# Kernel optimization log

Measured on AMD Instinct MI355X. Metric: run time of the kernel, lower is better.

Reference implementation:

```python
import jax, jax.numpy as jnp
import numpy as np

N = 8192
FIN = 128
FOUT = 64
NEG_BIG = -9e15


def setup_inputs() -> dict:
    key = jax.random.key(0)
    k1, k2, k3, k4 = jax.random.split(key, 4)
    x = jax.random.normal(k1, (N, FIN), dtype=jnp.float32)
    adj = jax.random.randint(k2, (N, N), 0, 2, dtype=jnp.int32)
    stdv_w = 1.0 / np.sqrt(FOUT)
    W = jax.random.uniform(k3, (FIN, FOUT), dtype=jnp.float32, minval=-stdv_w, maxval=stdv_w)
    # weight2: stdv = 1/sqrt(1) = 1
    a = jax.random.uniform(k4, (2 * FOUT, 1), dtype=jnp.float32, minval=-1.0, maxval=1.0)
    return {"x": x, "adj": adj, "W": W, "a": a}


def reference(x, adj, W, a):
    # h = x W  -> [N, Fout]
    h = x @ W
    # e_ij = relu(a^T [h_i || h_j]) decomposed exactly: a1.h_i + a2.h_j
    a1 = a[:FOUT, 0]  # [Fout]
    a2 = a[FOUT:, 0]  # [Fout]
    s1 = h @ a1  # [N]
    s2 = h @ a2  # [N]
    e = jax.nn.relu(s1[:, None] + s2[None, :])  # [N, N]
    att_logits = jnp.where(adj > 0, e, jnp.float32(NEG_BIG))
    attention = jax.nn.softmax(att_logits, axis=-1)  # [N, N]
    # dropout omitted (eval mode / p applied only in training)
    out = attention @ h  # [N, Fout]
    return out[None]  # [1, N, Fout] matching batch_size=1 reshape
```

## Files before the change

### kernel.cpp

```cpp
#include <hip/hip_runtime.h>
#include <cstdint>
#include <cstddef>

#define NN 8192
#define FIN 128
#define FOUT 64
#define BM 32
#define BN 64
#define JSPLIT 4
#define JCH (NN / JSPLIT)
#define NCHUNK (JCH / BN)
#define LDP 72

typedef __bf16 bf16x8 __attribute__((ext_vector_type(8)));
typedef unsigned short u16x8 __attribute__((ext_vector_type(8)));
typedef float f32x4 __attribute__((ext_vector_type(4)));

__device__ __forceinline__ unsigned short f2bf(float f) {
    unsigned u = __float_as_uint(f);
    u += 0x7FFFu + ((u >> 16) & 1u);
    return (unsigned short)(u >> 16);
}
__device__ __forceinline__ float bf2f(unsigned short b) {
    return __uint_as_float(((unsigned)b) << 16);
}

__global__ __launch_bounds__(256) void gat_prep(
    const float* __restrict__ x, const float* __restrict__ W,
    const float* __restrict__ a, float* __restrict__ s1,
    float* __restrict__ s2, unsigned short* __restrict__ Ht,
    unsigned int* __restrict__ s2max_enc)
{
    __shared__ __align__(16) float Wt[FOUT][FIN + 4];
    __shared__ float wa1[FIN], wa2[FIN];
    __shared__ float ash[2 * FOUT];
    __shared__ float s2sh[BM];

    const int tid = threadIdx.x;
    const int i0 = blockIdx.x * BM;

    for (int it = 0; it < 32; ++it) {
        int idx = it * 256 + tid;
        int k = idx >> 6, t = idx & 63;
        Wt[t][k] = W[idx];
    }
    if (tid < 2 * FOUT) ash[tid] = a[tid];
    __syncthreads();

    if (tid < FIN) {
        int k = tid;
        float acc = 0.f;
        #pragma unroll 8
        for (int t = 0; t < FOUT; ++t) acc = fmaf(Wt[t][k], ash[t], acc);
        wa1[k] = acc;
    } else {
        int k = tid - FIN;
        float acc = 0.f;
        #pragma unroll 8
        for (int t = 0; t < FOUT; ++t) acc = fmaf(Wt[t][k], ash[FOUT + t], acc);
        wa2[k] = acc;
    }
    __syncthreads();

    {
        int r = tid >> 3;
        int seg = tid & 7;
        const float* xp = x + (size_t)(i0 + r) * FIN + seg * 16;
        float d1 = 0.f, d2 = 0.f;
        #pragma unroll
        for (int m = 0; m < 16; ++m) {
            float xv = xp[m];
            d1 = fmaf(xv, wa1[seg * 16 + m], d1);
            d2 = fmaf(xv, wa2[seg * 16 + m], d2);
        }
        #pragma unroll
        for (int mk = 1; mk < 8; mk <<= 1) {
            d1 += __shfl_xor(d1, mk);
            d2 += __shfl_xor(d2, mk);
        }
        if (seg == 0) {
            s1[i0 + r] = d1;
            s2[i0 + r] = d2;
            s2sh[r] = d2;
        }
    }

    {
        const int lane = tid & 63;
        const int wv = tid >> 6;
        const int ih = wv & 1, nh = wv >> 1;
        const int m = lane & 15, quad = lane >> 4;
        f32x4 hacc0 = {0.f, 0.f, 0.f, 0.f};
        f32x4 hacc1 = {0.f, 0.f, 0.f, 0.f};
        const float* xrow = x + (size_t)(i0 + ih * 16 + m) * FIN + quad * 8;
        #pragma unroll
        for (int ks = 0; ks < 4; ++ks) {
            const float* xp = xrow + ks * 32;
            u16x8 ua;
            #pragma unroll
            for (int jj = 0; jj < 8; ++jj) ua[jj] = f2bf(xp[jj]);
            bf16x8 af = __builtin_bit_cast(bf16x8, ua);
            {
                const float* wp = &Wt[nh * 32 + m][ks * 32 + quad * 8];
                u16x8 ub;
                #pragma unroll
                for (int jj = 0; jj < 8; ++jj) ub[jj] = f2bf(wp[jj]);
                bf16x8 bfr = __builtin_bit_cast(bf16x8, ub);
                hacc0 = __builtin_amdgcn_mfma_f32_16x16x32_bf16(af, bfr, hacc0, 0, 0, 0);
            }
            {
                const float* wp = &Wt[nh * 32 + 16 + m][ks * 32 + quad * 8];
                u16x8 ub;
                #pragma unroll
                for (int jj = 0; jj < 8; ++jj) ub[jj] = f2bf(wp[jj]);
                bf16x8 bfr = __builtin_bit_cast(bf16x8, ub);
                hacc1 = __builtin_amdgcn_mfma_f32_16x16x32_bf16(af, bfr, hacc1, 0, 0, 0);
            }
        }
        #pragma unroll
        for (int reg = 0; reg < 4; ++reg) {
            int irow = i0 + ih * 16 + quad * 4 + reg;
            int t0 = nh * 32 + m;
            Ht[(size_t)t0 * NN + irow] = f2bf(hacc0[reg]);
            Ht[(size_t)(t0 + 16) * NN + irow] = f2bf(hacc1[reg]);
        }
    }
    __syncthreads();
    if (tid == 0) {
        float mx = s2sh[0];
        #pragma unroll
        for (int r = 1; r < BM; ++r) mx = fmaxf(mx, s2sh[r]);
        unsigned ub = __float_as_uint(mx);
        unsigned enc = (ub & 0x80000000u) ? ~ub : (ub | 0x80000000u);
        atomicMax(s2max_enc, enc);
    }
}

__global__ __launch_bounds__(256, 4) void gat_attn(
    const int* __restrict__ adj, const float* __restrict__ s1,
    const float* __restrict__ s2, const unsigned short* __restrict__ Ht,
    const unsigned int* __restrict__ s2max_enc,
    float* __restrict__ pacc, float* __restrict__ pl)
{
    __shared__ __align__(16) unsigned short p_lds[BM][LDP];
    __shared__ __align__(16) unsigned short ht_lds[FOUT][LDP];
    __shared__ float s1v[BM], Mv[BM], lrow[BM];

    const int tid = threadIdx.x;
    const int bx = blockIdx.x;
    const int r = bx >> 2;
    const int js = bx & 3;
    const int i0 = r * BM;
    const int j0 = js * JCH;

    {
        unsigned u = *s2max_enc;
        float S2MAX = (u & 0x80000000u) ? __uint_as_float(u ^ 0x80000000u)
                                        : __uint_as_float(~u);
        if (tid < BM) {
            float s = s1[i0 + tid];
            s1v[tid] = s;
            Mv[tid] = fmaxf(0.f, s + S2MAX);
            lrow[tid] = 0.f;
        }
    }
    __syncthreads();

    const int li = tid >> 4;
    const int jg = (tid & 15) * 4;
    const int th = tid >> 3;
    const int jh = (tid & 7) * 8;

    const int* adjp0 = adj + (size_t)(i0 + li) * NN + j0 + jg;
    const int* adjp1 = adjp0 + 16 * NN;
    const unsigned short* htp0 = Ht + (size_t)th * NN + j0 + jh;
    const unsigned short* htp1 = htp0 + 32 * NN;

    const int lane = tid & 63;
    const int wv = tid >> 6;
    const int ih = wv & 1, nh = wv >> 1;
    const int cm = lane & 15, quad = lane >> 4;

    f32x4 acc0 = {0.f, 0.f, 0.f, 0.f};
    f32x4 acc1 = {0.f, 0.f, 0.f, 0.f};

    int4 ca0 = *(const int4*)adjp0;
    int4 ca1 = *(const int4*)adjp1;
    uint4 ch0 = *(const uint4*)htp0;
    uint4 ch1 = *(const uint4*)htp1;

    const float s1a = s1v[li], Ma = Mv[li];
    const float s1b = s1v[li + 16], Mb = Mv[li + 16];

    for (int c = 0; c < NCHUNK; ++c) {
        const int cn = (c + 1 < NCHUNK) ? (c + 1) : c;
        int4 na0 = *(const int4*)(adjp0 + cn * BN);
        int4 na1 = *(const int4*)(adjp1 + cn * BN);
        uint4 nh0 = *(const uint4*)(htp0 + cn * BN);
        uint4 nh1 = *(const uint4*)(htp1 + cn * BN);

        __syncthreads();

        *(uint4*)&ht_lds[th][jh] = ch0;
        *(uint4*)&ht_lds[th + 32][jh] = ch1;

        {
            const float4 s2q = *(const float4*)(s2 + j0 + c * BN + jg);
            const int* av0 = (const int*)&ca0;
            const int* av1 = (const int*)&ca1;
            const float* s2v = (const float*)&s2q;
            unsigned short qa[4], qb[4];
            float psA = 0.f, psB = 0.f;
            #pragma unroll
            for (int jj = 0; jj < 4; ++jj) {
                float s2x = s2v[jj];
                float eA = fmaxf(s1a + s2x, 0.f);
                float pA = (av0[jj] > 0) ? __expf(eA - Ma) : 0.f;
                qa[jj] = f2bf(pA);
                psA += bf2f(qa[jj]);
                float eB = fmaxf(s1b + s2x, 0.f);
                float pB = (av1[jj] > 0) ? __expf(eB - Mb) : 0.f;
                qb[jj] = f2bf(pB);
                psB += bf2f(qb[jj]);
            }
            *(ushort4*)&p_lds[li][jg]      = make_ushort4(qa[0], qa[1], qa[2], qa[3]);
            *(ushort4*)&p_lds[li + 16][jg] = make_ushort4(qb[0], qb[1], qb[2], qb[3]);
            #pragma unroll
            for (int mk = 1; mk < 16; mk <<= 1) {
                psA += __shfl_xor(psA, mk);
                psB += __shfl_xor(psB, mk);
            }
            if ((tid & 15) == 0) {
                lrow[li] += psA;
                lrow[li + 16] += psB;
            }
        }
        __syncthreads();

        #pragma unroll
        for (int ks = 0; ks < 2; ++ks) {
            bf16x8 af  = *(const bf16x8*)&p_lds[ih * 16 + cm][ks * 32 + quad * 8];
            bf16x8 bf0 = *(const bf16x8*)&ht_lds[nh * 32 + cm][ks * 32 + quad * 8];
            bf16x8 bf1 = *(const bf16x8*)&ht_lds[nh * 32 + 16 + cm][ks * 32 + quad * 8];
            acc0 = __builtin_amdgcn_mfma_f32_16x16x32_bf16(af, bf0, acc0, 0, 0, 0);
            acc1 = __builtin_amdgcn_mfma_f32_16x16x32_bf16(af, bf1, acc1, 0, 0, 0);
        }

        ca0 = na0; ca1 = na1; ch0 = nh0; ch1 = nh1;
    }
    __syncthreads();

    #pragma unroll
    for (int reg = 0; reg < 4; ++reg) {
        int irow = i0 + ih * 16 + quad * 4 + reg;
        int n0 = nh * 32 + cm;
        pacc[((size_t)js * NN + irow) * FOUT + n0]      = acc0[reg];
        pacc[((size_t)js * NN + irow) * FOUT + n0 + 16] = acc1[reg];
    }
    if (tid < BM) pl[(size_t)js * NN + i0 + tid] = lrow[tid];
}

__global__ __launch_bounds__(256) void gat_combine(
    const float* __restrict__ pacc, const float* __restrict__ pl,
    float* __restrict__ out)
{
    int idx = blockIdx.x * 256 + threadIdx.x;
    int i = idx >> 6;
    float s = 0.f, l = 0.f;
    #pragma unroll
    for (int js = 0; js < JSPLIT; ++js) {
        s += pacc[(size_t)js * NN * FOUT + idx];
        l += pl[(size_t)js * NN + i];
    }
    out[idx] = s / l;
}

extern "C" void kernel_launch(void* const* d_in, const int* in_sizes, int n_in,
                              void* d_out, int out_size, void* d_ws, size_t ws_size,
                              hipStream_t stream) {
    const float* x   = (const float*)d_in[0];
    const int*   adj = (const int*)d_in[1];
    const float* W   = (const float*)d_in[2];
    const float* a   = (const float*)d_in[3];
    float* out = (float*)d_out;

    char* ws = (char*)d_ws;
    float* s1             = (float*)(ws);
    float* s2             = (float*)(ws + 32768);
    unsigned int* s2enc   = (unsigned int*)(ws + 65536);
    unsigned short* Ht    = (unsigned short*)(ws + 66560);
    float* pacc           = (float*)(ws + 66560 + 1048576);
    float* pl             = (float*)(ws + 66560 + 1048576 + 8388608);

    hipMemsetAsync(s2enc, 0, 4, stream);
    gat_prep<<<NN / BM, 256, 0, stream>>>(x, W, a, s1, s2, Ht, s2enc);
    gat_attn<<<(NN / BM) * JSPLIT, 256, 0, stream>>>(adj, s1, s2, Ht, s2enc, pacc, pl);
    gat_combine<<<NN * FOUT / 256, 256, 0, stream>>>(pacc, pl, out);
}
```

Before: 403.0 us.

## Double-buffer LDS tiles to drop a barrier, stage s2 in LDS, defer row-sum reduction

Double-buffers the P and H tiles in shared memory, which removes one of the two __syncthreads per chunk. The block's s2 slice is staged in LDS once at the start instead of being read from global memory every chunk. The per-chunk shuffle reduction and LDS accumulation of row sums become per-thread register accumulation, reduced once at the end. The cost is more LDS per block (the extra buffer plus 8KB for s2), which could lower occupancy against the 4-blocks launch bound.

```diff
diff --git a/kernel.cpp b/kernel.cpp
--- a/kernel.cpp
+++ b/kernel.cpp
@@ -142,9 +142,10 @@
     const unsigned int* __restrict__ s2max_enc,
     float* __restrict__ pacc, float* __restrict__ pl)
 {
-    __shared__ __align__(16) unsigned short p_lds[BM][LDP];
-    __shared__ __align__(16) unsigned short ht_lds[FOUT][LDP];
-    __shared__ float s1v[BM], Mv[BM], lrow[BM];
+    __shared__ __align__(16) unsigned short p_lds[2][BM][LDP];
+    __shared__ __align__(16) unsigned short ht_lds[2][FOUT][LDP];
+    __shared__ __align__(16) float s2sh[JCH];
+    __shared__ float s1v[BM], Mv[BM];
 
     const int tid = threadIdx.x;
     const int bx = blockIdx.x;
@@ -153,7 +154,27 @@
     const int i0 = r * BM;
     const int j0 = js * JCH;
 
+    const int li = tid >> 4;
+    const int jg = (tid & 15) * 4;
+    const int th = tid >> 3;
+    const int jh = (tid & 7) * 8;
+
+    const int* adjp0 = adj + (size_t)(i0 + li) * NN + j0 + jg;
+    const int* adjp1 = adjp0 + 16 * NN;
+    const unsigned short* htp0 = Ht + (size_t)th * NN + j0 + jh;
+    const unsigned short* htp1 = htp0 + 32 * NN;
+
+    int4 ca0 = *(const int4*)adjp0;
+    int4 ca1 = *(const int4*)adjp1;
+    uint4 ch0 = *(const uint4*)htp0;
+    uint4 ch1 = *(const uint4*)htp1;
+
     {
+        #pragma unroll
+        for (int it = 0; it < 2; ++it) {
+            int idx = (it * 256 + tid) * 4;
+            *(float4*)&s2sh[idx] = *(const float4*)(s2 + j0 + idx);
+        }
         unsigned u = *s2max_enc;
         float S2MAX = (u & 0x80000000u) ? __uint_as_float(u ^ 0x80000000u)
                                         : __uint_as_float(~u);
@@ -161,20 +182,9 @@
             float s = s1[i0 + tid];
             s1v[tid] = s;
             Mv[tid] = fmaxf(0.f, s + S2MAX);
-            lrow[tid] = 0.f;
         }
     }
     __syncthreads();
-
-    const int li = tid >> 4;
-    const int jg = (tid & 15) * 4;
-    const int th = tid >> 3;
-    const int jh = (tid & 7) * 8;
-
-    const int* adjp0 = adj + (size_t)(i0 + li) * NN + j0 + jg;
-    const int* adjp1 = adjp0 + 16 * NN;
-    const unsigned short* htp0 = Ht + (size_t)th * NN + j0 + jh;
-    const unsigned short* htp1 = htp0 + 32 * NN;
 
     const int lane = tid & 63;
     const int wv = tid >> 6;
@@ -183,34 +193,28 @@
 
     f32x4 acc0 = {0.f, 0.f, 0.f, 0.f};
     f32x4 acc1 = {0.f, 0.f, 0.f, 0.f};
-
-    int4 ca0 = *(const int4*)adjp0;
-    int4 ca1 = *(const int4*)adjp1;
-    uint4 ch0 = *(const uint4*)htp0;
-    uint4 ch1 = *(const uint4*)htp1;
+    float psA = 0.f, psB = 0.f;
 
     const float s1a = s1v[li], Ma = Mv[li];
     const float s1b = s1v[li + 16], Mb = Mv[li + 16];
 
     for (int c = 0; c < NCHUNK; ++c) {
+        const int buf = c & 1;
+
         const int cn = (c + 1 < NCHUNK) ? (c + 1) : c;
         int4 na0 = *(const int4*)(adjp0 + cn * BN);
         int4 na1 = *(const int4*)(adjp1 + cn * BN);
         uint4 nh0 = *(const uint4*)(htp0 + cn * BN);
         uint4 nh1 = *(const uint4*)(htp1 + cn * BN);
 
-        __syncthreads();
-
-        *(uint4*)&ht_lds[th][jh] = ch0;
-        *(uint4*)&ht_lds[th + 32][jh] = ch1;
+        *(uint4*)&ht_lds[buf][th][jh] = ch0;
+        *(uint4*)&ht_lds[buf][th + 32][jh] = ch1;
 
         {
-            const float4 s2q = *(const float4*)(s2 + j0 + c * BN + jg);
             const int* av0 = (const int*)&ca0;
             const int* av1 = (const int*)&ca1;
-            const float* s2v = (const float*)&s2q;
+            const float* s2v = &s2sh[c * BN + jg];
             unsigned short qa[4], qb[4];
-            float psA = 0.f, psB = 0.f;
             #pragma unroll
             for (int jj = 0; jj < 4; ++jj) {
                 float s2x = s2v[jj];
@@ -223,32 +227,33 @@
                 qb[jj] = f2bf(pB);
                 psB += bf2f(qb[jj]);
             }
-            *(ushort4*)&p_lds[li][jg]      = make_ushort4(qa[0], qa[1], qa[2], qa[3]);
-            *(ushort4*)&p_lds[li + 16][jg] = make_ushort4(qb[0], qb[1], qb[2], qb[3]);
-            #pragma unroll
-            for (int mk = 1; mk < 16; mk <<= 1) {
-                psA += __shfl_xor(psA, mk);
-                psB += __shfl_xor(psB, mk);
-            }
-            if ((tid & 15) == 0) {
-                lrow[li] += psA;
-                lrow[li + 16] += psB;
-            }
-        }
+            *(ushort4*)&p_lds[buf][li][jg]      = make_ushort4(qa[0], qa[1], qa[2], qa[3]);
+            *(ushort4*)&p_lds[buf][li + 16][jg] = make_ushort4(qb[0], qb[1], qb[2], qb[3]);
+        }
+
         __syncthreads();
 
         #pragma unroll
         for (int ks = 0; ks < 2; ++ks) {
-            bf16x8 af  = *(const bf16x8*)&p_lds[ih * 16 + cm][ks * 32 + quad * 8];
-            bf16x8 bf0 = *(const bf16x8*)&ht_lds[nh * 32 + cm][ks * 32 + quad * 8];
-            bf16x8 bf1 = *(const bf16x8*)&ht_lds[nh * 32 + 16 + cm][ks * 32 + quad * 8];
+            bf16x8 af  = *(const bf16x8*)&p_lds[buf][ih * 16 + cm][ks * 32 + quad * 8];
+            bf16x8 bf0 = *(const bf16x8*)&ht_lds[buf][nh * 32 + cm][ks * 32 + quad * 8];
+            bf16x8 bf1 = *(const bf16x8*)&ht_lds[buf][nh * 32 + 16 + cm][ks * 32 + quad * 8];
             acc0 = __builtin_amdgcn_mfma_f32_16x16x32_bf16(af, bf0, acc0, 0, 0, 0);
             acc1 = __builtin_amdgcn_mfma_f32_16x16x32_bf16(af, bf1, acc1, 0, 0, 0);
         }
 
         ca0 = na0; ca1 = na1; ch0 = nh0; ch1 = nh1;
     }
-    __syncthreads();
+
+    #pragma unroll
+    for (int mk = 1; mk < 16; mk <<= 1) {
+        psA += __shfl_xor(psA, mk);
+        psB += __shfl_xor(psB, mk);
+    }
+    if ((tid & 15) == 0) {
+        pl[(size_t)js * NN + i0 + li]      = psA;
+        pl[(size_t)js * NN + i0 + li + 16] = psB;
+    }
 
     #pragma unroll
     for (int reg = 0; reg < 4; ++reg) {
@@ -257,7 +262,6 @@
         pacc[((size_t)js * NN + irow) * FOUT + n0]      = acc0[reg];
         pacc[((size_t)js * NN + irow) * FOUT + n0 + 16] = acc1[reg];
     }
-    if (tid < BM) pl[(size_t)js * NN + i0 + tid] = lrow[tid];
 }
 
 __global__ __launch_bounds__(256) void gat_combine(
```

After: 402.5 us. Within noise of the previous version (-0.1%).
